# Kernel optimization log

Measured on AMD Instinct MI355X. Metric: run time of the kernel, lower is better.

## Reference

```python
import jax, jax.numpy as jnp
import numpy as np

MAX_ITERS = 20
TOL = 1e-3


def best_fit_transform(A, B):
    # A, B: [N, m]; returns homogeneous transform T mapping A -> B.
    m = A.shape[1]
    cA = jnp.mean(A, axis=0)
    cB = jnp.mean(B, axis=0)
    AA = A - cA
    BB = B - cB
    H = AA.T @ BB                      # [m, m] cross-covariance
    U, S, Vt = jnp.linalg.svd(H)
    # reflection fix: if det(R) < 0, flip last row of Vt
    R0 = Vt.T @ U.T
    flip = jnp.linalg.det(R0) < 0
    Vt = Vt.at[m - 1].multiply(jnp.where(flip, -1.0, 1.0).astype(Vt.dtype))
    R = Vt.T @ U.T
    t = cB - R @ cA
    T = jnp.eye(m + 1, dtype=A.dtype).at[:m, :m].set(R).at[:m, m].set(t)
    return T, R, t


def nearest_neighbor(src, dst):
    # src, dst: [N, m]; brute-force 1-NN of each src point in dst.
    d2 = (jnp.sum(src * src, axis=1)[:, None]
          - 2.0 * (src @ dst.T)
          + jnp.sum(dst * dst, axis=1)[None, :])        # [N, N]
    idx = jnp.argmin(d2, axis=1)                          # [N]
    dmin = jnp.take_along_axis(d2, idx[:, None], axis=1)[:, 0]
    dist = jnp.sqrt(jnp.maximum(dmin, 0.0) + 1e-12)
    return dist, idx


def icp(A, B, max_iterations=MAX_ITERS, tolerance=TOL):
    m = A.shape[1]
    N = A.shape[0]
    src0 = jnp.concatenate([A.T, jnp.ones((1, N), A.dtype)], axis=0)  # [m+1, N]

    def step(carry, _):
        src, prev_err, done = carry
        dist, idx = nearest_neighbor(src[:m].T, B)
        T, _, _ = best_fit_transform(src[:m].T, B[idx])
        new_src = T @ src
        err = jnp.mean(dist)
        converged = jnp.abs(prev_err - err) < tolerance
        src = jnp.where(done, src, new_src)
        prev_err = jnp.where(done, prev_err, err)
        done = done | converged
        return (src, prev_err, done), None

    carry0 = (src0, jnp.zeros((), A.dtype), jnp.zeros((), bool))
    (src, _, _), _ = jax.lax.scan(step, carry0, None, length=max_iterations)
    T, _, _ = best_fit_transform(A, src[:m].T)
    return T


def setup_inputs() -> dict:
    key = jax.random.key(0)
    kA, kB = jax.random.split(key)
    A = jax.random.normal(kA, (8192, 3), dtype=jnp.float32)
    B = jax.random.normal(kB, (8192, 3), dtype=jnp.float32)
    return {"A": A, "B": B}


def reference(A, B):
    return icp(A, B)
```

## Files before the change

### kernel.cpp

```cpp
#include <hip/hip_runtime.h>

#define NPTS   8192
#define NB     256
#define NT     256
#define SRCW   8
#define NG8    16
#define MAXIT  20
#define TOLER  1e-3
#define SPINCAP 200000000u

typedef unsigned long long u64;
typedef unsigned int u32;
typedef float f2 __attribute__((ext_vector_type(2)));
typedef double dbl2 __attribute__((ext_vector_type(2)));

#define WS_PART    0
#define WS_FLAGS   65536

__device__ inline double atom_ld(const double* p) {
  return __hip_atomic_load(p, __ATOMIC_RELAXED, __HIP_MEMORY_SCOPE_AGENT);
}
__device__ inline void atom_st(double* p, double v) {
  __hip_atomic_store(p, v, __ATOMIC_RELAXED, __HIP_MEMORY_SCOPE_AGENT);
}
__device__ inline int atom_ldi(const int* p) {
  return __hip_atomic_load(p, __ATOMIC_RELAXED, __HIP_MEMORY_SCOPE_AGENT);
}
__device__ inline void atom_sti(int* p, int v) {
  __hip_atomic_store(p, v, __ATOMIC_RELAXED, __HIP_MEMORY_SCOPE_AGENT);
}

__device__ void eig3f(const float K[3][3], float w[3], float V[3][3])
{
  const float p1 = K[0][1]*K[0][1] + K[0][2]*K[0][2] + K[1][2]*K[1][2];
  const float q  = (K[0][0] + K[1][1] + K[2][2]) * (1.f/3.f);
  const float p2 = (K[0][0]-q)*(K[0][0]-q) + (K[1][1]-q)*(K[1][1]-q)
                 + (K[2][2]-q)*(K[2][2]-q) + 2.f*p1;
  if (p2 < 1e-20f) {
    w[0]=w[1]=w[2]=q;
    V[0][0]=1;V[1][0]=0;V[2][0]=0; V[0][1]=0;V[1][1]=1;V[2][1]=0;
    V[0][2]=0;V[1][2]=0;V[2][2]=1;
    return;
  }
  const float p = sqrtf(p2 * (1.f/6.f));
  const float ip = 1.f / p;
  float Bm[3][3];
  for (int i = 0; i < 3; ++i)
    for (int j = 0; j < 3; ++j)
      Bm[i][j] = (K[i][j] - ((i==j) ? q : 0.f)) * ip;
  float detB = Bm[0][0]*(Bm[1][1]*Bm[2][2] - Bm[1][2]*Bm[2][1])
             - Bm[0][1]*(Bm[1][0]*Bm[2][2] - Bm[1][2]*Bm[2][0])
             + Bm[0][2]*(Bm[1][0]*Bm[2][1] - Bm[1][1]*Bm[2][0]);
  float r = fminf(1.f, fmaxf(-1.f, detB * 0.5f));
  const float phi = acosf(r) * (1.f/3.f);
  w[0] = q + 2.f*p*cosf(phi);
  w[2] = q + 2.f*p*cosf(phi + 2.0943951023931953f);
  w[1] = 3.f*q - w[0] - w[2];
  for (int kk = 0; kk < 2; ++kk) {
    const int k = (kk == 0) ? 0 : 2;
    float lam = w[k];
    float r0[3] = {K[0][0]-lam, K[0][1], K[0][2]};
    float r1[3] = {K[1][0], K[1][1]-lam, K[1][2]};
    float r2[3] = {K[2][0], K[2][1], K[2][2]-lam};
    float c01[3] = {r0[1]*r1[2]-r0[2]*r1[1], r0[2]*r1[0]-r0[0]*r1[2], r0[0]*r1[1]-r0[1]*r1[0]};
    float c12[3] = {r1[1]*r2[2]-r1[2]*r2[1], r1[2]*r2[0]-r1[0]*r2[2], r1[0]*r2[1]-r1[1]*r2[0]};
    float c20[3] = {r2[1]*r0[2]-r2[2]*r0[1], r2[2]*r0[0]-r2[0]*r0[2], r2[0]*r0[1]-r2[1]*r0[0]};
    float n01 = c01[0]*c01[0]+c01[1]*c01[1]+c01[2]*c01[2];
    float n12 = c12[0]*c12[0]+c12[1]*c12[1]+c12[2]*c12[2];
    float n20 = c20[0]*c20[0]+c20[1]*c20[1]+c20[2]*c20[2];
    float* best = c01; float nb = n01;
    if (n12 > nb) { best = c12; nb = n12; }
    if (n20 > nb) { best = c20; nb = n20; }
    float inv = 1.f / sqrtf(nb + 1e-30f);
    V[0][k]=best[0]*inv; V[1][k]=best[1]*inv; V[2][k]=best[2]*inv;
  }
  V[0][1] = V[1][2]*V[2][0] - V[2][2]*V[1][0];
  V[1][1] = V[2][2]*V[0][0] - V[0][2]*V[2][0];
  V[2][1] = V[0][2]*V[1][0] - V[1][2]*V[0][0];
  float nm = sqrtf(V[0][1]*V[0][1]+V[1][1]*V[1][1]+V[2][1]*V[2][1]) + 1e-30f;
  V[0][1] /= nm; V[1][1] /= nm; V[2][1] /= nm;
}

__device__ void kabsch_Rf(const float H[3][3], float R[3][3])
{
  float K[3][3];
  for (int i = 0; i < 3; ++i)
    for (int j = 0; j < 3; ++j) {
      float s = 0.f;
      for (int k = 0; k < 3; ++k) s += H[k][i] * H[k][j];
      K[i][j] = s;
    }
  float w[3], V[3][3];
  eig3f(K, w, V);
  float U[3][3];
  for (int k = 0; k < 3; ++k) {
    float u0 = H[0][0]*V[0][k] + H[0][1]*V[1][k] + H[0][2]*V[2][k];
    float u1 = H[1][0]*V[0][k] + H[1][1]*V[1][k] + H[1][2]*V[2][k];
    float u2 = H[2][0]*V[0][k] + H[2][1]*V[1][k] + H[2][2]*V[2][k];
    float n = sqrtf(u0*u0 + u1*u1 + u2*u2);
    if (n > 1e-18f) { u0 /= n; u1 /= n; u2 /= n; }
    else if (k == 2) {
      u0 = U[1][0]*U[2][1] - U[2][0]*U[1][1];
      u1 = U[2][0]*U[0][1] - U[0][0]*U[2][1];
      u2 = U[0][0]*U[1][1] - U[1][0]*U[0][1];
      float n2 = sqrtf(u0*u0 + u1*u1 + u2*u2) + 1e-30f;
      u0 /= n2; u1 /= n2; u2 /= n2;
    } else {
      u0 = (k == 0) ? 1.f : 0.f; u1 = (k == 1) ? 1.f : 0.f; u2 = 0.f;
    }
    U[0][k] = u0; U[1][k] = u1; U[2][k] = u2;
  }
  float R0[3][3];
  for (int i = 0; i < 3; ++i)
    for (int j = 0; j < 3; ++j)
      R0[i][j] = V[i][0]*U[j][0] + V[i][1]*U[j][1] + V[i][2]*U[j][2];
  float det = R0[0][0]*(R0[1][1]*R0[2][2] - R0[1][2]*R0[2][1])
            - R0[0][1]*(R0[1][0]*R0[2][2] - R0[1][2]*R0[2][0])
            + R0[0][2]*(R0[1][0]*R0[2][1] - R0[1][1]*R0[2][0]);
  if (det < 0.f)
    for (int i = 0; i < 3; ++i)
      for (int j = 0; j < 3; ++j)
        R0[i][j] -= 2.f * V[i][2] * U[j][2];
  for (int i = 0; i < 3; ++i)
    for (int j = 0; j < 3; ++j)
      R[i][j] = R0[i][j];
}

__device__ inline void flag_barrier(int* flags, int blk, int gen,
                                    int tid, int wav, int lane)
{
  __syncthreads();
  if (tid == 0) {
    __threadfence();
    atom_sti(&flags[blk], gen);
  }
  if (wav == 0) {
    const int base = lane * 4;
    u32 spins = 0;
    bool ok = false;
    while (!ok && spins < SPINCAP) {
      int f0 = atom_ldi(&flags[base + 0]);
      int f1 = atom_ldi(&flags[base + 1]);
      int f2_ = atom_ldi(&flags[base + 2]);
      int f3 = atom_ldi(&flags[base + 3]);
      ok = __all((f0 >= gen) && (f1 >= gen) && (f2_ >= gen) && (f3 >= gen));
      if (!ok) __builtin_amdgcn_s_sleep(2);
      ++spins;
    }
  }
  __syncthreads();
  __threadfence();
}

__global__ __launch_bounds__(NT, 1)
void icp_all(const float* __restrict__ A, const float* __restrict__ B,
             char* __restrict__ ws, float* __restrict__ out)
{
  double* partials = (double*)(ws + WS_PART);
  int*    flags    = (int*)(ws + WS_FLAGS);

  __shared__ __align__(16) float4 bp_lds[NPTS];
  __shared__ __align__(16) double red1[32 * 16];
  __shared__ double red2[4 * 16];
  __shared__ float  Tl[12];
  __shared__ int    dl;

  const int tid  = threadIdx.x;
  const int blk  = blockIdx.x;
  const int wav  = tid >> 6;
  const int lane = tid & 63;
  const int qbase = blk * 32 + wav * SRCW;

  for (int i = tid; i < NPTS; i += NT) {
    float bx = B[3*i], by = B[3*i+1], bz = B[3*i+2];
    bp_lds[i] = make_float4(2.f*bx, 2.f*by, 2.f*bz, bx*bx + by*by + bz*bz);
  }

  float ax[8], ay[8], az[8], sx[8], sy[8], sz[8];
  #pragma unroll
  for (int i = 0; i < 8; ++i) {
    int p = qbase + i;
    ax[i] = A[3*p]; ay[i] = A[3*p+1]; az[i] = A[3*p+2];
    sx[i] = ax[i];  sy[i] = ay[i];    sz[i] = az[i];
  }
  __syncthreads();

  double prev_err = 0.0;
  int it = 0;
  for (; it < MAXIT; ++it) {
    const int par = it & 1;
    f2 nsx2[4], nsy2[4], nsz2[4];
    #pragma unroll
    for (int k = 0; k < 4; ++k) {
      f2 vx = { -sx[2*k], -sx[2*k+1] };
      f2 vy = { -sy[2*k], -sy[2*k+1] };
      f2 vz = { -sz[2*k], -sz[2*k+1] };
      nsx2[k] = vx; nsy2[k] = vy; nsz2[k] = vz;
    }

    float emin[8]; int gmin[8];
    #pragma unroll
    for (int i = 0; i < 8; ++i) { emin[i] = 3.4e38f; gmin[i] = 0; }

    float4 dd[8];
    #pragma unroll
    for (int m = 0; m < 8; ++m) dd[m] = bp_lds[m * 64 + lane];

    for (int g = 0; g < NG8 - 1; ++g) {
      f2 run[4];
      #pragma unroll
      for (int m = 0; m < 8; ++m) {
        f2 dx2 = { dd[m].x, dd[m].x };
        f2 dy2 = { dd[m].y, dd[m].y };
        f2 dz2 = { dd[m].z, dd[m].z };
        f2 dw2 = { dd[m].w, dd[m].w };
        #pragma unroll
        for (int k = 0; k < 4; ++k) {
          f2 e2 = __builtin_elementwise_fma(nsx2[k], dx2,
                   __builtin_elementwise_fma(nsy2[k], dy2,
                    __builtin_elementwise_fma(nsz2[k], dz2, dw2)));
          run[k] = (m == 0) ? e2 : __builtin_elementwise_min(run[k], e2);
        }
        dd[m] = bp_lds[(g + 1) * 512 + m * 64 + lane];
      }
      #pragma unroll
      for (int k = 0; k < 4; ++k) {
        if (run[k].x < emin[2*k])   gmin[2*k]   = g;
        emin[2*k]   = fminf(emin[2*k],   run[k].x);
        if (run[k].y < emin[2*k+1]) gmin[2*k+1] = g;
        emin[2*k+1] = fminf(emin[2*k+1], run[k].y);
      }
    }
    {
      const int g = NG8 - 1;
      f2 run[4];
      #pragma unroll
      for (int m = 0; m < 8; ++m) {
        f2 dx2 = { dd[m].x, dd[m].x };
        f2 dy2 = { dd[m].y, dd[m].y };
        f2 dz2 = { dd[m].z, dd[m].z };
        f2 dw2 = { dd[m].w, dd[m].w };
        #pragma unroll
        for (int k = 0; k < 4; ++k) {
          f2 e2 = __builtin_elementwise_fma(nsx2[k], dx2,
                   __builtin_elementwise_fma(nsy2[k], dy2,
                    __builtin_elementwise_fma(nsz2[k], dz2, dw2)));
          run[k] = (m == 0) ? e2 : __builtin_elementwise_min(run[k], e2);
        }
      }
      #pragma unroll
      for (int k = 0; k < 4; ++k) {
        if (run[k].x < emin[2*k])   gmin[2*k]   = g;
        emin[2*k]   = fminf(emin[2*k],   run[k].x);
        if (run[k].y < emin[2*k+1]) gmin[2*k+1] = g;
        emin[2*k+1] = fminf(emin[2*k+1], run[k].y);
      }
    }

    int meta[8];
    #pragma unroll
    for (int i = 0; i < 8; ++i) meta[i] = (gmin[i] << 6) | lane;
    #pragma unroll
    for (int m = 1; m < 64; m <<= 1) {
      #pragma unroll
      for (int i = 0; i < 8; ++i) {
        float eo = __shfl_xor(emin[i], m, 64);
        int   mo = __shfl_xor(meta[i], m, 64);
        if (eo < emin[i] || (eo == emin[i] && mo < meta[i])) { emin[i] = eo; meta[i] = mo; }
      }
    }

    {
      const int isrc = lane >> 3;
      float em = emin[0]; int mt = meta[0];
      float sxi = sx[0], syi = sy[0], szi = sz[0];
      #pragma unroll
      for (int k = 1; k < 8; ++k) {
        const bool p = (isrc == k);
        em  = p ? emin[k] : em;   mt  = p ? meta[k] : mt;
        sxi = p ? sx[k]  : sxi;   syi = p ? sy[k]  : syi;   szi = p ? sz[k] : szi;
      }
      const int gg = mt >> 6, ll = mt & 63;
      const int j0 = gg * 512 + ll;
      int jj = j0;
      #pragma unroll
      for (int m = 7; m >= 0; --m) {
        float4 c = bp_lds[j0 + m * 64];
        float e = fmaf(-sxi, c.x, fmaf(-syi, c.y, fmaf(-szi, c.z, c.w)));
        jj = (e == em) ? (j0 + m * 64) : jj;
      }
      float4 dmt = bp_lds[jj];
      const float bxm = 0.5f*dmt.x, bym = 0.5f*dmt.y, bzm = 0.5f*dmt.z;
      const double dsx = (double)sxi, dsy = (double)syi, dsz = (double)szi;
      const double dbx = (double)bxm, dby = (double)bym, dbz = (double)bzm;
      double w0, w1;
      switch (lane & 7) {
        case 0: w0 = dsx;       w1 = dsy;       break;
        case 1: w0 = dsz;       w1 = dbx;       break;
        case 2: w0 = dby;       w1 = dbz;       break;
        case 3: w0 = dsx * dbx; w1 = dsx * dby; break;
        case 4: w0 = dsx * dbz; w1 = dsy * dbx; break;
        case 5: w0 = dsy * dby; w1 = dsy * dbz; break;
        case 6: w0 = dsz * dbx; w1 = dsz * dby; break;
        default: {
          const float s2 = sxi*sxi + syi*syi + szi*szi;
          const float d2f = em + s2;
          w0 = dsz * dbz;
          w1 = (double)sqrtf(fmaxf(d2f, 0.f) + 1e-12f);
        } break;
      }
      dbl2 wv = { w0, w1 };
      *(dbl2*)&red1[(wav * 8 + isrc) * 16 + (lane & 7) * 2] = wv;
    }

    {
      const int k16 = lane & 15, h = lane >> 4;
      double s = red1[(wav*8 + h)*16 + k16] + red1[(wav*8 + 4 + h)*16 + k16];
      s += __shfl_xor(s, 16, 64);
      s += __shfl_xor(s, 32, 64);
      if (lane < 16) red2[wav * 16 + k16] = s;
    }
    __syncthreads();
    if (tid < 16) {
      double ssum = red2[tid] + red2[16 + tid] + red2[32 + tid] + red2[48 + tid];
      atom_st(&partials[((size_t)par * 16 + tid) * NB + blk], ssum);
    }
    flag_barrier(flags, blk, it + 1, tid, wav, lane);

    {
      double s0, s1, s2, s3;
      #pragma unroll
      for (int j = 0; j < 4; ++j) {
        const int k = wav * 4 + j;
        const double* row = &partials[((size_t)par * 16 + k) * NB + lane * 4];
        double t0 = atom_ld(row + 0), t1 = atom_ld(row + 1);
        double t2 = atom_ld(row + 2), t3 = atom_ld(row + 3);
        double s = ((t0 + t1) + (t2 + t3));
        #pragma unroll
        for (int m = 1; m < 64; m <<= 1) s += __shfl_xor(s, m, 64);
        if (j == 0) s0 = s; else if (j == 1) s1 = s;
        else if (j == 2) s2 = s; else s3 = s;
      }
      if (lane < 4) {
        double v = (lane == 0) ? s0 : (lane == 1) ? s1 : (lane == 2) ? s2 : s3;
        red2[wav * 4 + lane] = v;
      }
    }
    __syncthreads();
    if (tid == 0) {
      double S[16];
      for (int k = 0; k < 16; ++k) S[k] = red2[k];
      const double invN = 1.0 / NPTS;
      double cAv[3] = {S[0]*invN, S[1]*invN, S[2]*invN};
      double cBv[3] = {S[3]*invN, S[4]*invN, S[5]*invN};
      float H[3][3];
      for (int i = 0; i < 3; ++i)
        for (int j = 0; j < 3; ++j)
          H[i][j] = (float)(S[6 + i*3 + j] - (double)NPTS * cAv[i] * cBv[j]);
      double err = S[15] * invN;
      int conv = (fabs(prev_err - err) < TOLER) ? 1 : 0;
      prev_err = err;
      float R[3][3];
      kabsch_Rf(H, R);
      float t0 = (float)cBv[0] - (R[0][0]*(float)cAv[0] + R[0][1]*(float)cAv[1] + R[0][2]*(float)cAv[2]);
      float t1 = (float)cBv[1] - (R[1][0]*(float)cAv[0] + R[1][1]*(float)cAv[1] + R[1][2]*(float)cAv[2]);
      float t2 = (float)cBv[2] - (R[2][0]*(float)cAv[0] + R[2][1]*(float)cAv[1] + R[2][2]*(float)cAv[2]);
      Tl[0]=R[0][0]; Tl[1]=R[0][1]; Tl[2]=R[0][2];
      Tl[3]=R[1][0]; Tl[4]=R[1][1]; Tl[5]=R[1][2];
      Tl[6]=R[2][0]; Tl[7]=R[2][1]; Tl[8]=R[2][2];
      Tl[9]=t0; Tl[10]=t1; Tl[11]=t2;
      dl = conv;
    }
    __syncthreads();
    {
      float r00=Tl[0],r01=Tl[1],r02=Tl[2],r10=Tl[3],r11=Tl[4],r12=Tl[5];
      float r20=Tl[6],r21=Tl[7],r22=Tl[8],t0=Tl[9],t1=Tl[10],t2=Tl[11];
      int done = dl;
      #pragma unroll
      for (int i = 0; i < 8; ++i) {
        float nx = r00*sx[i] + r01*sy[i] + r02*sz[i] + t0;
        float ny = r10*sx[i] + r11*sy[i] + r12*sz[i] + t1;
        float nz = r20*sx[i] + r21*sy[i] + r22*sz[i] + t2;
        sx[i]=nx; sy[i]=ny; sz[i]=nz;
      }
      if (done) break;
    }
  }

  const int fpar = (it < MAXIT) ? ((it + 1) & 1) : (MAXIT & 1);
  const int fgen = (it < MAXIT) ? (it + 2) : (MAXIT + 1);
  {
    const int isrc = lane >> 3;
    float axi = ax[0], ayi = ay[0], azi = az[0];
    float sxi = sx[0], syi = sy[0], szi = sz[0];
    #pragma unroll
    for (int k = 1; k < 8; ++k) {
      const bool p = (isrc == k);
      axi = p ? ax[k] : axi;  ayi = p ? ay[k] : ayi;  azi = p ? az[k] : azi;
      sxi = p ? sx[k] : sxi;  syi = p ? sy[k] : syi;  szi = p ? sz[k] : szi;
    }
    const double dax = (double)axi, day = (double)ayi, daz = (double)azi;
    const double dsx = (double)sxi, dsy = (double)syi, dsz = (double)szi;
    double w0, w1;
    switch (lane & 7) {
      case 0: w0 = dax;       w1 = day;       break;
      case 1: w0 = daz;       w1 = dsx;       break;
      case 2: w0 = dsy;       w1 = dsz;       break;
      case 3: w0 = dax * dsx; w1 = dax * dsy; break;
      case 4: w0 = dax * dsz; w1 = day * dsx; break;
      case 5: w0 = day * dsy; w1 = day * dsz; break;
      case 6: w0 = daz * dsx; w1 = daz * dsy; break;
      default: w0 = daz * dsz; w1 = 0.0;      break;
    }
    dbl2 wv = { w0, w1 };
    *(dbl2*)&red1[(wav * 8 + isrc) * 16 + (lane & 7) * 2] = wv;
  }
  {
    const int k16 = lane & 15, h = lane >> 4;
    double s = red1[(wav*8 + h)*16 + k16] + red1[(wav*8 + 4 + h)*16 + k16];
    s += __shfl_xor(s, 16, 64);
    s += __shfl_xor(s, 32, 64);
    if (lane < 16) red2[wav * 16 + k16] = s;
  }
  __syncthreads();
  if (tid < 16) {
    double ssum = red2[tid] + red2[16 + tid] + red2[32 + tid] + red2[48 + tid];
    atom_st(&partials[((size_t)fpar * 16 + tid) * NB + blk], ssum);
  }
  if (blk != 0) {
    __syncthreads();
    if (tid == 0) { __threadfence(); atom_sti(&flags[blk], fgen); }
    return;
  }
  flag_barrier(flags, blk, fgen, tid, wav, lane);

  double a2[16];
  #pragma unroll
  for (int k = 0; k < 16; ++k)
    a2[k] = atom_ld(&partials[((size_t)fpar * 16 + k) * NB + tid]);
  for (int m = 1; m < 64; m <<= 1) {
    #pragma unroll
    for (int k = 0; k < 16; ++k) a2[k] += __shfl_xor(a2[k], m, 64);
  }
  if (lane == 0)
    for (int k = 0; k < 16; ++k) red2[wav * 16 + k] = a2[k];
  __syncthreads();
  if (tid == 0) {
    double S[16];
    for (int k = 0; k < 16; ++k)
      S[k] = red2[k] + red2[16+k] + red2[32+k] + red2[48+k];
    const double invN = 1.0 / NPTS;
    double cAv[3] = {S[0]*invN, S[1]*invN, S[2]*invN};
    double cSv[3] = {S[3]*invN, S[4]*invN, S[5]*invN};
    float H[3][3];
    for (int i = 0; i < 3; ++i)
      for (int j = 0; j < 3; ++j)
        H[i][j] = (float)(S[6 + i*3 + j] - (double)NPTS * cAv[i] * cSv[j]);
    float R[3][3];
    kabsch_Rf(H, R);
    float u0 = (float)cSv[0] - (R[0][0]*(float)cAv[0] + R[0][1]*(float)cAv[1] + R[0][2]*(float)cAv[2]);
    float u1 = (float)cSv[1] - (R[1][0]*(float)cAv[0] + R[1][1]*(float)cAv[1] + R[1][2]*(float)cAv[2]);
    float u2 = (float)cSv[2] - (R[2][0]*(float)cAv[0] + R[2][1]*(float)cAv[1] + R[2][2]*(float)cAv[2]);
    out[0]=R[0][0]; out[1]=R[0][1]; out[2]=R[0][2]; out[3]=u0;
    out[4]=R[1][0]; out[5]=R[1][1]; out[6]=R[1][2]; out[7]=u1;
    out[8]=R[2][0]; out[9]=R[2][1]; out[10]=R[2][2]; out[11]=u2;
    out[12]=0.f; out[13]=0.f; out[14]=0.f; out[15]=1.f;
  }
}

extern "C" void kernel_launch(void* const* d_in, const int* in_sizes, int n_in,
                              void* d_out, int out_size, void* d_ws, size_t ws_size,
                              hipStream_t stream) {
  const float* A = (const float*)d_in[0];
  const float* B = (const float*)d_in[1];
  float* out = (float*)d_out;
  char* ws = (char*)d_ws;

  hipLaunchKernelGGL(icp_all, dim3(NB), dim3(NT), 0, stream, A, B, ws, out);
}
```

Baseline: 141.7 us.

## Double threads per block, halve source points per wave in NN search

Raises block size from 256 to 512 threads while each wave now handles 4 source points instead of 8. Each block keeps its 32 source points, so the per-wave brute-force scan of all B points is spread over twice as many waves, which shortens the per-iteration critical path. The argmin reduction is restructured to shuffle per-point first and then across lanes, and the final reduction is reworked to use the two-row-per-wave pattern. The cost is that every wave rereads the full LDS copy of B for only 4 points, doubling LDS traffic per source point, and the block barrier now spans 8 waves.

```diff
diff --git a/kernel.cpp b/kernel.cpp
--- a/kernel.cpp
+++ b/kernel.cpp
@@ -2,8 +2,8 @@
 
 #define NPTS   8192
 #define NB     256
-#define NT     256
-#define SRCW   8
+#define NT     512
+#define SRCW   4
 #define NG8    16
 #define MAXIT  20
 #define TOLER  1e-3
@@ -161,7 +161,7 @@
 
   __shared__ __align__(16) float4 bp_lds[NPTS];
   __shared__ __align__(16) double red1[32 * 16];
-  __shared__ double red2[4 * 16];
+  __shared__ double red2[8 * 16];
   __shared__ float  Tl[12];
   __shared__ int    dl;
 
@@ -176,9 +176,9 @@
     bp_lds[i] = make_float4(2.f*bx, 2.f*by, 2.f*bz, bx*bx + by*by + bz*bz);
   }
 
-  float ax[8], ay[8], az[8], sx[8], sy[8], sz[8];
+  float ax[4], ay[4], az[4], sx[4], sy[4], sz[4];
   #pragma unroll
-  for (int i = 0; i < 8; ++i) {
+  for (int i = 0; i < 4; ++i) {
     int p = qbase + i;
     ax[i] = A[3*p]; ay[i] = A[3*p+1]; az[i] = A[3*p+2];
     sx[i] = ax[i];  sy[i] = ay[i];    sz[i] = az[i];
@@ -189,25 +189,25 @@
   int it = 0;
   for (; it < MAXIT; ++it) {
     const int par = it & 1;
-    f2 nsx2[4], nsy2[4], nsz2[4];
-    #pragma unroll
-    for (int k = 0; k < 4; ++k) {
+    f2 nsx2[2], nsy2[2], nsz2[2];
+    #pragma unroll
+    for (int k = 0; k < 2; ++k) {
       f2 vx = { -sx[2*k], -sx[2*k+1] };
       f2 vy = { -sy[2*k], -sy[2*k+1] };
       f2 vz = { -sz[2*k], -sz[2*k+1] };
       nsx2[k] = vx; nsy2[k] = vy; nsz2[k] = vz;
     }
 
-    float emin[8]; int gmin[8];
-    #pragma unroll
-    for (int i = 0; i < 8; ++i) { emin[i] = 3.4e38f; gmin[i] = 0; }
+    float emin[4]; int gmin[4];
+    #pragma unroll
+    for (int i = 0; i < 4; ++i) { emin[i] = 3.4e38f; gmin[i] = 0; }
 
     float4 dd[8];
     #pragma unroll
     for (int m = 0; m < 8; ++m) dd[m] = bp_lds[m * 64 + lane];
 
     for (int g = 0; g < NG8 - 1; ++g) {
-      f2 run[4];
+      f2 run[2];
       #pragma unroll
       for (int m = 0; m < 8; ++m) {
         f2 dx2 = { dd[m].x, dd[m].x };
@@ -215,7 +215,7 @@
         f2 dz2 = { dd[m].z, dd[m].z };
         f2 dw2 = { dd[m].w, dd[m].w };
         #pragma unroll
-        for (int k = 0; k < 4; ++k) {
+        for (int k = 0; k < 2; ++k) {
           f2 e2 = __builtin_elementwise_fma(nsx2[k], dx2,
                    __builtin_elementwise_fma(nsy2[k], dy2,
                     __builtin_elementwise_fma(nsz2[k], dz2, dw2)));
@@ -224,7 +224,7 @@
         dd[m] = bp_lds[(g + 1) * 512 + m * 64 + lane];
       }
       #pragma unroll
-      for (int k = 0; k < 4; ++k) {
+      for (int k = 0; k < 2; ++k) {
         if (run[k].x < emin[2*k])   gmin[2*k]   = g;
         emin[2*k]   = fminf(emin[2*k],   run[k].x);
         if (run[k].y < emin[2*k+1]) gmin[2*k+1] = g;
@@ -233,7 +233,7 @@
     }
     {
       const int g = NG8 - 1;
-      f2 run[4];
+      f2 run[2];
       #pragma unroll
       for (int m = 0; m < 8; ++m) {
         f2 dx2 = { dd[m].x, dd[m].x };
@@ -241,7 +241,7 @@
         f2 dz2 = { dd[m].z, dd[m].z };
         f2 dw2 = { dd[m].w, dd[m].w };
         #pragma unroll
-        for (int k = 0; k < 4; ++k) {
+        for (int k = 0; k < 2; ++k) {
           f2 e2 = __builtin_elementwise_fma(nsx2[k], dx2,
                    __builtin_elementwise_fma(nsy2[k], dy2,
                     __builtin_elementwise_fma(nsz2[k], dz2, dw2)));
@@ -249,7 +249,7 @@
         }
       }
       #pragma unroll
-      for (int k = 0; k < 4; ++k) {
+      for (int k = 0; k < 2; ++k) {
         if (run[k].x < emin[2*k])   gmin[2*k]   = g;
         emin[2*k]   = fminf(emin[2*k],   run[k].x);
         if (run[k].y < emin[2*k+1]) gmin[2*k+1] = g;
@@ -257,29 +257,37 @@
       }
     }
 
-    int meta[8];
-    #pragma unroll
-    for (int i = 0; i < 8; ++i) meta[i] = (gmin[i] << 6) | lane;
-    #pragma unroll
-    for (int m = 1; m < 64; m <<= 1) {
-      #pragma unroll
-      for (int i = 0; i < 8; ++i) {
+    int meta[4];
+    #pragma unroll
+    for (int i = 0; i < 4; ++i) meta[i] = (gmin[i] << 6) | lane;
+    #pragma unroll
+    for (int m = 1; m < 4; m <<= 1) {
+      #pragma unroll
+      for (int i = 0; i < 4; ++i) {
         float eo = __shfl_xor(emin[i], m, 64);
         int   mo = __shfl_xor(meta[i], m, 64);
         if (eo < emin[i] || (eo == emin[i] && mo < meta[i])) { emin[i] = eo; meta[i] = mo; }
       }
     }
+    const int isrc = lane & 3;
+    float em = emin[0]; int mt = meta[0];
+    float sxi = sx[0], syi = sy[0], szi = sz[0];
+    float axi = ax[0], ayi = ay[0], azi = az[0];
+    #pragma unroll
+    for (int k = 1; k < 4; ++k) {
+      const bool p = (isrc == k);
+      em  = p ? emin[k] : em;   mt  = p ? meta[k] : mt;
+      sxi = p ? sx[k]  : sxi;   syi = p ? sy[k]  : syi;   szi = p ? sz[k] : szi;
+      axi = p ? ax[k]  : axi;   ayi = p ? ay[k]  : ayi;   azi = p ? az[k] : azi;
+    }
+    #pragma unroll
+    for (int m = 4; m < 64; m <<= 1) {
+      float eo = __shfl_xor(em, m, 64);
+      int   mo = __shfl_xor(mt, m, 64);
+      if (eo < em || (eo == em && mo < mt)) { em = eo; mt = mo; }
+    }
 
     {
-      const int isrc = lane >> 3;
-      float em = emin[0]; int mt = meta[0];
-      float sxi = sx[0], syi = sy[0], szi = sz[0];
-      #pragma unroll
-      for (int k = 1; k < 8; ++k) {
-        const bool p = (isrc == k);
-        em  = p ? emin[k] : em;   mt  = p ? meta[k] : mt;
-        sxi = p ? sx[k]  : sxi;   syi = p ? sy[k]  : syi;   szi = p ? sz[k] : szi;
-      }
       const int gg = mt >> 6, ll = mt & 63;
       const int j0 = gg * 512 + ll;
       int jj = j0;
@@ -291,60 +299,60 @@
       }
       float4 dmt = bp_lds[jj];
       const float bxm = 0.5f*dmt.x, bym = 0.5f*dmt.y, bzm = 0.5f*dmt.z;
-      const double dsx = (double)sxi, dsy = (double)syi, dsz = (double)szi;
-      const double dbx = (double)bxm, dby = (double)bym, dbz = (double)bzm;
-      double w0, w1;
-      switch (lane & 7) {
-        case 0: w0 = dsx;       w1 = dsy;       break;
-        case 1: w0 = dsz;       w1 = dbx;       break;
-        case 2: w0 = dby;       w1 = dbz;       break;
-        case 3: w0 = dsx * dbx; w1 = dsx * dby; break;
-        case 4: w0 = dsx * dbz; w1 = dsy * dbx; break;
-        case 5: w0 = dsy * dby; w1 = dsy * dbz; break;
-        case 6: w0 = dsz * dbx; w1 = dsz * dby; break;
-        default: {
-          const float s2 = sxi*sxi + syi*syi + szi*szi;
-          const float d2f = em + s2;
-          w0 = dsz * dbz;
-          w1 = (double)sqrtf(fmaxf(d2f, 0.f) + 1e-12f);
-        } break;
-      }
-      dbl2 wv = { w0, w1 };
-      *(dbl2*)&red1[(wav * 8 + isrc) * 16 + (lane & 7) * 2] = wv;
+      if (lane < 32) {
+        const int ps = lane >> 2;
+        const double dsx = (double)sxi, dsy = (double)syi, dsz = (double)szi;
+        const double dbx = (double)bxm, dby = (double)bym, dbz = (double)bzm;
+        double w0, w1;
+        switch (ps) {
+          case 0: w0 = dsx;       w1 = dsy;       break;
+          case 1: w0 = dsz;       w1 = dbx;       break;
+          case 2: w0 = dby;       w1 = dbz;       break;
+          case 3: w0 = dsx * dbx; w1 = dsx * dby; break;
+          case 4: w0 = dsx * dbz; w1 = dsy * dbx; break;
+          case 5: w0 = dsy * dby; w1 = dsy * dbz; break;
+          case 6: w0 = dsz * dbx; w1 = dsz * dby; break;
+          default: {
+            const float s2 = sxi*sxi + syi*syi + szi*szi;
+            const float d2f = em + s2;
+            w0 = dsz * dbz;
+            w1 = (double)sqrtf(fmaxf(d2f, 0.f) + 1e-12f);
+          } break;
+        }
+        dbl2 wv = { w0, w1 };
+        *(dbl2*)&red1[(wav * 4 + isrc) * 16 + ps * 2] = wv;
+      }
     }
 
     {
       const int k16 = lane & 15, h = lane >> 4;
-      double s = red1[(wav*8 + h)*16 + k16] + red1[(wav*8 + 4 + h)*16 + k16];
+      double s = red1[(wav*4 + h)*16 + k16];
       s += __shfl_xor(s, 16, 64);
       s += __shfl_xor(s, 32, 64);
       if (lane < 16) red2[wav * 16 + k16] = s;
     }
     __syncthreads();
     if (tid < 16) {
-      double ssum = red2[tid] + red2[16 + tid] + red2[32 + tid] + red2[48 + tid];
+      double ssum = red2[tid] + red2[16+tid] + red2[32+tid] + red2[48+tid]
+                  + red2[64+tid] + red2[80+tid] + red2[96+tid] + red2[112+tid];
       atom_st(&partials[((size_t)par * 16 + tid) * NB + blk], ssum);
     }
     flag_barrier(flags, blk, it + 1, tid, wav, lane);
 
     {
-      double s0, s1, s2, s3;
-      #pragma unroll
-      for (int j = 0; j < 4; ++j) {
-        const int k = wav * 4 + j;
+      double s0, s1;
+      #pragma unroll
+      for (int j = 0; j < 2; ++j) {
+        const int k = wav * 2 + j;
         const double* row = &partials[((size_t)par * 16 + k) * NB + lane * 4];
         double t0 = atom_ld(row + 0), t1 = atom_ld(row + 1);
         double t2 = atom_ld(row + 2), t3 = atom_ld(row + 3);
         double s = ((t0 + t1) + (t2 + t3));
         #pragma unroll
         for (int m = 1; m < 64; m <<= 1) s += __shfl_xor(s, m, 64);
-        if (j == 0) s0 = s; else if (j == 1) s1 = s;
-        else if (j == 2) s2 = s; else s3 = s;
-      }
-      if (lane < 4) {
-        double v = (lane == 0) ? s0 : (lane == 1) ? s1 : (lane == 2) ? s2 : s3;
-        red2[wav * 4 + lane] = v;
-      }
+        if (j == 0) s0 = s; else s1 = s;
+      }
+      if (lane == 0) { red2[wav*2 + 0] = s0; red2[wav*2 + 1] = s1; }
     }
     __syncthreads();
     if (tid == 0) {
@@ -377,7 +385,7 @@
       float r20=Tl[6],r21=Tl[7],r22=Tl[8],t0=Tl[9],t1=Tl[10],t2=Tl[11];
       int done = dl;
       #pragma unroll
-      for (int i = 0; i < 8; ++i) {
+      for (int i = 0; i < 4; ++i) {
         float nx = r00*sx[i] + r01*sy[i] + r02*sz[i] + t0;
         float ny = r10*sx[i] + r11*sy[i] + r12*sz[i] + t1;
         float nz = r20*sx[i] + r21*sy[i] + r22*sz[i] + t2;
@@ -390,41 +398,45 @@
   const int fpar = (it < MAXIT) ? ((it + 1) & 1) : (MAXIT & 1);
   const int fgen = (it < MAXIT) ? (it + 2) : (MAXIT + 1);
   {
-    const int isrc = lane >> 3;
+    const int isrc = lane & 3;
     float axi = ax[0], ayi = ay[0], azi = az[0];
     float sxi = sx[0], syi = sy[0], szi = sz[0];
     #pragma unroll
-    for (int k = 1; k < 8; ++k) {
+    for (int k = 1; k < 4; ++k) {
       const bool p = (isrc == k);
       axi = p ? ax[k] : axi;  ayi = p ? ay[k] : ayi;  azi = p ? az[k] : azi;
       sxi = p ? sx[k] : sxi;  syi = p ? sy[k] : syi;  szi = p ? sz[k] : szi;
     }
-    const double dax = (double)axi, day = (double)ayi, daz = (double)azi;
-    const double dsx = (double)sxi, dsy = (double)syi, dsz = (double)szi;
-    double w0, w1;
-    switch (lane & 7) {
-      case 0: w0 = dax;       w1 = day;       break;
-      case 1: w0 = daz;       w1 = dsx;       break;
-      case 2: w0 = dsy;       w1 = dsz;       break;
-      case 3: w0 = dax * dsx; w1 = dax * dsy; break;
-      case 4: w0 = dax * dsz; w1 = day * dsx; break;
-      case 5: w0 = day * dsy; w1 = day * dsz; break;
-      case 6: w0 = daz * dsx; w1 = daz * dsy; break;
-      default: w0 = daz * dsz; w1 = 0.0;      break;
-    }
-    dbl2 wv = { w0, w1 };
-    *(dbl2*)&red1[(wav * 8 + isrc) * 16 + (lane & 7) * 2] = wv;
+    if (lane < 32) {
+      const int ps = lane >> 2;
+      const double dax = (double)axi, day = (double)ayi, daz = (double)azi;
+      const double dsx = (double)sxi, dsy = (double)syi, dsz = (double)szi;
+      double w0, w1;
+      switch (ps) {
+        case 0: w0 = dax;       w1 = day;       break;
+        case 1: w0 = daz;       w1 = dsx;       break;
+        case 2: w0 = dsy;       w1 = dsz;       break;
+        case 3: w0 = dax * dsx; w1 = dax * dsy; break;
+        case 4: w0 = dax * dsz; w1 = day * dsx; break;
+        case 5: w0 = day * dsy; w1 = day * dsz; break;
+        case 6: w0 = daz * dsx; w1 = daz * dsy; break;
+        default: w0 = daz * dsz; w1 = 0.0;      break;
+      }
+      dbl2 wv = { w0, w1 };
+      *(dbl2*)&red1[(wav * 4 + isrc) * 16 + ps * 2] = wv;
+    }
   }
   {
     const int k16 = lane & 15, h = lane >> 4;
-    double s = red1[(wav*8 + h)*16 + k16] + red1[(wav*8 + 4 + h)*16 + k16];
+    double s = red1[(wav*4 + h)*16 + k16];
     s += __shfl_xor(s, 16, 64);
     s += __shfl_xor(s, 32, 64);
     if (lane < 16) red2[wav * 16 + k16] = s;
   }
   __syncthreads();
   if (tid < 16) {
-    double ssum = red2[tid] + red2[16 + tid] + red2[32 + tid] + red2[48 + tid];
+    double ssum = red2[tid] + red2[16+tid] + red2[32+tid] + red2[48+tid]
+                + red2[64+tid] + red2[80+tid] + red2[96+tid] + red2[112+tid];
     atom_st(&partials[((size_t)fpar * 16 + tid) * NB + blk], ssum);
   }
   if (blk != 0) {
@@ -434,21 +446,25 @@
   }
   flag_barrier(flags, blk, fgen, tid, wav, lane);
 
-  double a2[16];
-  #pragma unroll
-  for (int k = 0; k < 16; ++k)
-    a2[k] = atom_ld(&partials[((size_t)fpar * 16 + k) * NB + tid]);
-  for (int m = 1; m < 64; m <<= 1) {
-    #pragma unroll
-    for (int k = 0; k < 16; ++k) a2[k] += __shfl_xor(a2[k], m, 64);
-  }
-  if (lane == 0)
-    for (int k = 0; k < 16; ++k) red2[wav * 16 + k] = a2[k];
+  {
+    double s0, s1;
+    #pragma unroll
+    for (int j = 0; j < 2; ++j) {
+      const int k = wav * 2 + j;
+      const double* row = &partials[((size_t)fpar * 16 + k) * NB + lane * 4];
+      double t0 = atom_ld(row + 0), t1 = atom_ld(row + 1);
+      double t2 = atom_ld(row + 2), t3 = atom_ld(row + 3);
+      double s = ((t0 + t1) + (t2 + t3));
+      #pragma unroll
+      for (int m = 1; m < 64; m <<= 1) s += __shfl_xor(s, m, 64);
+      if (j == 0) s0 = s; else s1 = s;
+    }
+    if (lane == 0) { red2[wav*2 + 0] = s0; red2[wav*2 + 1] = s1; }
+  }
   __syncthreads();
   if (tid == 0) {
     double S[16];
-    for (int k = 0; k < 16; ++k)
-      S[k] = red2[k] + red2[16+k] + red2[32+k] + red2[48+k];
+    for (int k = 0; k < 16; ++k) S[k] = red2[k];
     const double invN = 1.0 / NPTS;
     double cAv[3] = {S[0]*invN, S[1]*invN, S[2]*invN};
     double cSv[3] = {S[3]*invN, S[4]*invN, S[5]*invN};
```

Result: slower. 159.5 us (+12.6%).

## Split NN search across two waves per query group with 512-thread blocks

Applied to the files above, without the earlier changes.

Doubles the block to 512 threads, so each group of 8 query points is handled by two wavefronts that each scan half of the destination points. The halves are merged through shared memory before the moment reduction, and the cross-block partial reads are re-split across 8 waves. The aim is more latency hiding and a shorter per-wave serial scan per iteration. In exchange it adds extra __syncthreads and an LDS merge step, and leaves half the waves idle during the weight computation.

```diff
diff --git a/kernel.cpp b/kernel.cpp
--- a/kernel.cpp
+++ b/kernel.cpp
@@ -2,9 +2,9 @@
 
 #define NPTS   8192
 #define NB     256
-#define NT     256
-#define SRCW   8
+#define NT     512
 #define NG8    16
+#define HGRP   8
 #define MAXIT  20
 #define TOLER  1e-3
 #define SPINCAP 200000000u
@@ -161,7 +161,9 @@
 
   __shared__ __align__(16) float4 bp_lds[NPTS];
   __shared__ __align__(16) double red1[32 * 16];
-  __shared__ double red2[4 * 16];
+  __shared__ double red2[8 * 16];
+  __shared__ float  mE[8][8];
+  __shared__ int    mM[8][8];
   __shared__ float  Tl[12];
   __shared__ int    dl;
 
@@ -169,7 +171,10 @@
   const int blk  = blockIdx.x;
   const int wav  = tid >> 6;
   const int lane = tid & 63;
-  const int qbase = blk * 32 + wav * SRCW;
+  const int pr   = wav >> 1;
+  const int hh   = wav & 1;
+  const int qbase = blk * 32 + pr * 8;
+  const int dbase = hh * (HGRP * 512);
 
   for (int i = tid; i < NPTS; i += NT) {
     float bx = B[3*i], by = B[3*i+1], bz = B[3*i+2];
@@ -204,9 +209,9 @@
 
     float4 dd[8];
     #pragma unroll
-    for (int m = 0; m < 8; ++m) dd[m] = bp_lds[m * 64 + lane];
-
-    for (int g = 0; g < NG8 - 1; ++g) {
+    for (int m = 0; m < 8; ++m) dd[m] = bp_lds[dbase + m * 64 + lane];
+
+    for (int g = 0; g < HGRP - 1; ++g) {
       f2 run[4];
       #pragma unroll
       for (int m = 0; m < 8; ++m) {
@@ -221,7 +226,7 @@
                     __builtin_elementwise_fma(nsz2[k], dz2, dw2)));
           run[k] = (m == 0) ? e2 : __builtin_elementwise_min(run[k], e2);
         }
-        dd[m] = bp_lds[(g + 1) * 512 + m * 64 + lane];
+        dd[m] = bp_lds[dbase + (g + 1) * 512 + m * 64 + lane];
       }
       #pragma unroll
       for (int k = 0; k < 4; ++k) {
@@ -232,7 +237,7 @@
       }
     }
     {
-      const int g = NG8 - 1;
+      const int g = HGRP - 1;
       f2 run[4];
       #pragma unroll
       for (int m = 0; m < 8; ++m) {
@@ -259,7 +264,7 @@
 
     int meta[8];
     #pragma unroll
-    for (int i = 0; i < 8; ++i) meta[i] = (gmin[i] << 6) | lane;
+    for (int i = 0; i < 8; ++i) meta[i] = ((hh * HGRP + gmin[i]) << 6) | lane;
     #pragma unroll
     for (int m = 1; m < 64; m <<= 1) {
       #pragma unroll
@@ -270,7 +275,23 @@
       }
     }
 
-    {
+    if (lane < 8) {
+      float se = emin[0]; int sm = meta[0];
+      #pragma unroll
+      for (int k = 1; k < 8; ++k) {
+        const bool p = (lane == k);
+        se = p ? emin[k] : se;  sm = p ? meta[k] : sm;
+      }
+      mE[wav][lane] = se;  mM[wav][lane] = sm;
+    }
+    __syncthreads();
+
+    if (hh == 0) {
+      #pragma unroll
+      for (int i = 0; i < 8; ++i) {
+        float eo = mE[wav + 1][i]; int mo = mM[wav + 1][i];
+        if (eo < emin[i] || (eo == emin[i] && mo < meta[i])) { emin[i] = eo; meta[i] = mo; }
+      }
       const int isrc = lane >> 3;
       float em = emin[0]; int mt = meta[0];
       float sxi = sx[0], syi = sy[0], szi = sz[0];
@@ -310,41 +331,39 @@
         } break;
       }
       dbl2 wv = { w0, w1 };
-      *(dbl2*)&red1[(wav * 8 + isrc) * 16 + (lane & 7) * 2] = wv;
-    }
+      *(dbl2*)&red1[(pr * 8 + isrc) * 16 + (lane & 7) * 2] = wv;
+    }
+    __syncthreads();
 
     {
-      const int k16 = lane & 15, h = lane >> 4;
-      double s = red1[(wav*8 + h)*16 + k16] + red1[(wav*8 + 4 + h)*16 + k16];
+      const int k16 = lane & 15, h2 = lane >> 4;
+      double s = red1[(wav*4 + h2)*16 + k16];
       s += __shfl_xor(s, 16, 64);
       s += __shfl_xor(s, 32, 64);
       if (lane < 16) red2[wav * 16 + k16] = s;
     }
     __syncthreads();
     if (tid < 16) {
-      double ssum = red2[tid] + red2[16 + tid] + red2[32 + tid] + red2[48 + tid];
+      double ssum = red2[tid] + red2[16+tid] + red2[32+tid] + red2[48+tid]
+                  + red2[64+tid] + red2[80+tid] + red2[96+tid] + red2[112+tid];
       atom_st(&partials[((size_t)par * 16 + tid) * NB + blk], ssum);
     }
     flag_barrier(flags, blk, it + 1, tid, wav, lane);
 
     {
-      double s0, s1, s2, s3;
-      #pragma unroll
-      for (int j = 0; j < 4; ++j) {
-        const int k = wav * 4 + j;
+      double s0, s1;
+      #pragma unroll
+      for (int j = 0; j < 2; ++j) {
+        const int k = wav * 2 + j;
         const double* row = &partials[((size_t)par * 16 + k) * NB + lane * 4];
         double t0 = atom_ld(row + 0), t1 = atom_ld(row + 1);
         double t2 = atom_ld(row + 2), t3 = atom_ld(row + 3);
         double s = ((t0 + t1) + (t2 + t3));
         #pragma unroll
         for (int m = 1; m < 64; m <<= 1) s += __shfl_xor(s, m, 64);
-        if (j == 0) s0 = s; else if (j == 1) s1 = s;
-        else if (j == 2) s2 = s; else s3 = s;
-      }
-      if (lane < 4) {
-        double v = (lane == 0) ? s0 : (lane == 1) ? s1 : (lane == 2) ? s2 : s3;
-        red2[wav * 4 + lane] = v;
-      }
+        if (j == 0) s0 = s; else s1 = s;
+      }
+      if (lane == 0) { red2[wav*2 + 0] = s0; red2[wav*2 + 1] = s1; }
     }
     __syncthreads();
     if (tid == 0) {
@@ -389,7 +408,7 @@
 
   const int fpar = (it < MAXIT) ? ((it + 1) & 1) : (MAXIT & 1);
   const int fgen = (it < MAXIT) ? (it + 2) : (MAXIT + 1);
-  {
+  if (hh == 0) {
     const int isrc = lane >> 3;
     float axi = ax[0], ayi = ay[0], azi = az[0];
     float sxi = sx[0], syi = sy[0], szi = sz[0];
@@ -413,18 +432,20 @@
       default: w0 = daz * dsz; w1 = 0.0;      break;
     }
     dbl2 wv = { w0, w1 };
-    *(dbl2*)&red1[(wav * 8 + isrc) * 16 + (lane & 7) * 2] = wv;
-  }
+    *(dbl2*)&red1[(pr * 8 + isrc) * 16 + (lane & 7) * 2] = wv;
+  }
+  __syncthreads();
   {
-    const int k16 = lane & 15, h = lane >> 4;
-    double s = red1[(wav*8 + h)*16 + k16] + red1[(wav*8 + 4 + h)*16 + k16];
+    const int k16 = lane & 15, h2 = lane >> 4;
+    double s = red1[(wav*4 + h2)*16 + k16];
     s += __shfl_xor(s, 16, 64);
     s += __shfl_xor(s, 32, 64);
     if (lane < 16) red2[wav * 16 + k16] = s;
   }
   __syncthreads();
   if (tid < 16) {
-    double ssum = red2[tid] + red2[16 + tid] + red2[32 + tid] + red2[48 + tid];
+    double ssum = red2[tid] + red2[16+tid] + red2[32+tid] + red2[48+tid]
+                + red2[64+tid] + red2[80+tid] + red2[96+tid] + red2[112+tid];
     atom_st(&partials[((size_t)fpar * 16 + tid) * NB + blk], ssum);
   }
   if (blk != 0) {
@@ -434,21 +455,25 @@
   }
   flag_barrier(flags, blk, fgen, tid, wav, lane);
 
-  double a2[16];
-  #pragma unroll
-  for (int k = 0; k < 16; ++k)
-    a2[k] = atom_ld(&partials[((size_t)fpar * 16 + k) * NB + tid]);
-  for (int m = 1; m < 64; m <<= 1) {
-    #pragma unroll
-    for (int k = 0; k < 16; ++k) a2[k] += __shfl_xor(a2[k], m, 64);
-  }
-  if (lane == 0)
-    for (int k = 0; k < 16; ++k) red2[wav * 16 + k] = a2[k];
+  {
+    double s0, s1;
+    #pragma unroll
+    for (int j = 0; j < 2; ++j) {
+      const int k = wav * 2 + j;
+      const double* row = &partials[((size_t)fpar * 16 + k) * NB + lane * 4];
+      double t0 = atom_ld(row + 0), t1 = atom_ld(row + 1);
+      double t2 = atom_ld(row + 2), t3 = atom_ld(row + 3);
+      double s = ((t0 + t1) + (t2 + t3));
+      #pragma unroll
+      for (int m = 1; m < 64; m <<= 1) s += __shfl_xor(s, m, 64);
+      if (j == 0) s0 = s; else s1 = s;
+    }
+    if (lane == 0) { red2[wav*2 + 0] = s0; red2[wav*2 + 1] = s1; }
+  }
   __syncthreads();
   if (tid == 0) {
     double S[16];
-    for (int k = 0; k < 16; ++k)
-      S[k] = red2[k] + red2[16+k] + red2[32+k] + red2[48+k];
+    for (int k = 0; k < 16; ++k) S[k] = red2[k];
     const double invN = 1.0 / NPTS;
     double cAv[3] = {S[0]*invN, S[1]*invN, S[2]*invN};
     double cSv[3] = {S[3]*invN, S[4]*invN, S[5]*invN};
```

Measured after the change: 166.6 us. +17.6%, slower.
